# Performance work log

Measured on AMD Instinct MI355X. Metric: run time of the kernel, lower is better.

## Reference

```python
import jax, jax.numpy as jnp
import numpy as np

T = 2048        # tokens (single prefill sequence)
H = 4096        # hidden size
NQ = 32         # query heads
NKV = 8         # kv heads
HD = 128        # qk head_dim
VD = 96         # v head_dim (mismatched -> pad/slice path)
WIN = 1024      # sliding window size
E = 8           # routed experts
F = 1408        # moe intermediate
K = 2           # experts per token
EPS = 1e-6
THETA = 1e6


def setup_inputs() -> dict:
    key = jax.random.key(0)
    ks = jax.random.split(key, 10)
    s = 0.02
    return {
        "positions": jnp.arange(T, dtype=jnp.int32),
        "hidden_states": jax.random.normal(ks[0], (T, H), jnp.float32),
        "rms1_w": jnp.ones((H,), jnp.float32),
        "rms2_w": jnp.ones((H,), jnp.float32),
        "wq": jax.random.normal(ks[1], (H, NQ * HD), jnp.float32) * s,
        "wk": jax.random.normal(ks[2], (H, NKV * HD), jnp.float32) * s,
        "wv": jax.random.normal(ks[3], (H, NKV * VD), jnp.float32) * s,
        "wo": jax.random.normal(ks[4], (NQ * VD, H), jnp.float32) * s,
        "sink": jax.random.normal(ks[5], (NQ,), jnp.float32),
        "gate_w": jax.random.normal(ks[6], (H, E), jnp.float32) * s,
        "w_gate": jax.random.normal(ks[7], (E, H, F), jnp.float32) * s,
        "w_up": jax.random.normal(ks[8], (E, H, F), jnp.float32) * s,
        "w_down": jax.random.normal(ks[9], (E, F, H), jnp.float32) * s,
    }


def _rmsnorm(x, w):
    var = jnp.mean(x * x, axis=-1, keepdims=True)
    return x * jax.lax.rsqrt(var + EPS) * w


def _rope(positions, x):
    # neox style, full rotary over HD
    inv_freq = 1.0 / (THETA ** (jnp.arange(0, HD, 2, dtype=jnp.float32) / HD))
    ang = positions.astype(jnp.float32)[:, None] * inv_freq      # [T, HD/2]
    cos = jnp.cos(ang)[:, None, :]                               # [T, 1, HD/2]
    sin = jnp.sin(ang)[:, None, :]
    x1, x2 = x[..., : HD // 2], x[..., HD // 2 :]
    return jnp.concatenate([x1 * cos - x2 * sin, x2 * cos + x1 * sin], axis=-1)


def _forward(positions, hidden_states, rms1_w, rms2_w, wq, wk, wv, wo, sink,
             gate_w, w_gate, w_up, w_down):
    residual = hidden_states
    x = _rmsnorm(hidden_states, rms1_w)

    # ---- attention ----
    q = (x @ wq).reshape(T, NQ, HD)
    k = (x @ wk).reshape(T, NKV, HD)
    v = (x @ wv).reshape(T, NKV, VD)
    q = _rope(positions, q)
    k = _rope(positions, k)
    rep = NQ // NKV
    k = jnp.repeat(k, rep, axis=1)   # [T, NQ, HD]
    v = jnp.repeat(v, rep, axis=1)   # [T, NQ, VD]

    scale = HD ** -0.5
    scores = jnp.einsum('qhd,khd->hqk', q, k) * scale           # [NQ, T, T]
    i = positions[:, None]
    j = positions[None, :]
    mask = (j <= i) & ((i - j) < WIN)                            # causal + sliding window
    scores = jnp.where(mask[None, :, :], scores, jnp.float32(-1e30))
    # attention sink: extra per-head logit contributing only to the denominator
    sink_col = jnp.broadcast_to(sink[:, None, None], (NQ, T, 1))
    logits = jnp.concatenate([scores, sink_col], axis=-1)        # [NQ, T, T+1]
    probs = jax.nn.softmax(logits, axis=-1)[..., :T]
    attn = jnp.einsum('hqk,khv->qhv', probs, v)                  # [T, NQ, VD]
    attn_out = attn.reshape(T, NQ * VD) @ wo                     # [T, H]

    h = residual + attn_out

    # ---- MoE FFN ----
    x2 = _rmsnorm(h, rms2_w)
    router_logits = x2 @ gate_w                                   # [T, E]
    router_probs = jax.nn.softmax(router_logits, axis=-1)
    topk_w, topk_ids = jax.lax.top_k(router_probs, K)             # [T, K]
    topk_w = topk_w / jnp.sum(topk_w, axis=-1, keepdims=True)     # renormalize
    combine = jnp.zeros((T, E), jnp.float32).at[
        jnp.arange(T)[:, None], topk_ids].add(topk_w)             # [T, E]

    h1 = jnp.einsum('td,edf->etf', x2, w_gate)
    h2 = jnp.einsum('td,edf->etf', x2, w_up)
    eo = jnp.einsum('etf,efd->etd', jax.nn.silu(h1) * h2, w_down)  # [E, T, H]
    moe_out = jnp.einsum('etd,te->td', eo, combine)               # [T, H]

    return h + moe_out


def reference(positions, hidden_states, rms1_w, rms2_w, wq, wk, wv, wo, sink,
              gate_w, w_gate, w_up, w_down):
    return _forward(positions, hidden_states, rms1_w, rms2_w, wq, wk, wv, wo,
                    sink, gate_w, w_gate, w_up, w_down)
```

## Files before the change

kernel.cpp:

```cpp
#include <hip/hip_runtime.h>
#include <math.h>

#define T 2048
#define H 4096
#define NQ 32
#define NKV 8
#define HD 128
#define VD 96
#define WIN 1024
#define NE 8
#define FF 1408
#define TOPK 2

typedef __bf16 bf16x8 __attribute__((ext_vector_type(8)));
typedef unsigned short u16x8 __attribute__((ext_vector_type(8)));
typedef float f32x4 __attribute__((ext_vector_type(4)));
typedef unsigned short ushort_t;

__device__ __forceinline__ unsigned short f2bf(float f) {
  union { float f; unsigned u; } v; v.f = f;
  unsigned r = v.u + 0x7fffu + ((v.u >> 16) & 1u);
  return (unsigned short)(r >> 16);
}
__device__ __forceinline__ float bf2f(unsigned short h) {
  union { unsigned u; float f; } v; v.u = ((unsigned)h) << 16;
  return v.f;
}
__device__ __forceinline__ f32x4 mfma16(bf16x8 a, bf16x8 b, f32x4 c) {
  return __builtin_amdgcn_mfma_f32_16x16x32_bf16(a, b, c, 0, 0, 0);
}
__device__ __forceinline__ f32x4 fzero4() { f32x4 z = {0.f, 0.f, 0.f, 0.f}; return z; }

__device__ __forceinline__ void gl16(const void* g, void* l) {
  __builtin_amdgcn_global_load_lds(
      (const __attribute__((address_space(1))) void*)g,
      (__attribute__((address_space(3))) void*)l, 16, 0, 0);
}

template<int SPLITOUT>
__global__ __launch_bounds__(256) void tconv_kernel(
    const float* __restrict__ src, int ldsrc,
    ushort_t* __restrict__ dh, ushort_t* __restrict__ dl,
    int lddst, int dro, long long sE, long long dE)
{
  __shared__ float tile[64][65];
  int e = blockIdx.z;
  src += sE * (long long)e;
  dh += dE * (long long)e;
  if (SPLITOUT) dl += dE * (long long)e;
  int c0 = blockIdx.x * 64;
  int r0 = blockIdx.y * 64;
  int tid = threadIdx.x;
#pragma unroll
  for (int i = 0; i < 4; ++i) {
    int idx = tid + i * 256;
    int r = idx >> 4, c4 = (idx & 15) << 2;
    float4 v = *(const float4*)&src[(size_t)(r0 + r) * ldsrc + c0 + c4];
    tile[r][c4 + 0] = v.x; tile[r][c4 + 1] = v.y;
    tile[r][c4 + 2] = v.z; tile[r][c4 + 3] = v.w;
  }
  __syncthreads();
#pragma unroll
  for (int i = 0; i < 2; ++i) {
    int idx = tid + i * 256;
    int c = idx >> 3, r8 = (idx & 7) << 3;
    u16x8 hv, lv;
#pragma unroll
    for (int j = 0; j < 8; ++j) {
      float f = tile[r8 + j][c];
      unsigned short hh = f2bf(f);
      hv[j] = hh;
      if (SPLITOUT) lv[j] = f2bf(f - bf2f(hh));
    }
    size_t o = (size_t)(dro + c0 + c) * lddst + r0 + r8;
    *(u16x8*)&dh[o] = hv;
    if (SPLITOUT) *(u16x8*)&dl[o] = lv;
  }
}

template<int SPLIT, int GATHER, int EOFF, int OUTBF, int RES>
__global__ __launch_bounds__(256) void gemm_bt(
    const ushort_t* __restrict__ Ah, const ushort_t* __restrict__ Al, int lda,
    const ushort_t* __restrict__ Bh, const ushort_t* __restrict__ Bl,
    long long strideBe,
    void* __restrict__ Cp, int ldc,
    const float* __restrict__ res,
    const int* __restrict__ row_idx, const int* __restrict__ e_off,
    int M, int K)
{
  __shared__ __align__(16) ushort_t As[(SPLIT ? 2 : 1) * 4096];
  __shared__ __align__(16) ushort_t Bs[(SPLIT ? 2 : 1) * 4096];

  int rowbase = 0, Mloc = M;
  if (EOFF) {
    int e = blockIdx.z;
    rowbase = e_off[e];
    Mloc = e_off[e + 1] - rowbase;
    Bh += strideBe * (long long)e;
    if (SPLIT) Bl += strideBe * (long long)e;
  }
  int mtile = blockIdx.y * 128;
  if (mtile >= Mloc) return;
  int n0 = blockIdx.x * 128;

  int tid = threadIdx.x;
  int lane = tid & 63, wave = tid >> 6;
  int g = lane >> 4, cc = lane & 15;
  int wrow = (wave >> 1) * 64, wcol = (wave & 1) * 64;

  int ks = (tid & 3) << 3;
  const ushort_t *aph0, *aph1, *apl0 = nullptr, *apl1 = nullptr;
  {
    int r0 = (tid >> 2), r1 = (tid >> 2) + 64;
    long long ar0, ar1;
    if (EOFF || GATHER) {
      int g0 = mtile + r0; if (g0 >= Mloc) g0 = 0;
      int g1 = mtile + r1; if (g1 >= Mloc) g1 = 0;
      if (GATHER) { ar0 = row_idx[rowbase + g0]; ar1 = row_idx[rowbase + g1]; }
      else { ar0 = rowbase + g0; ar1 = rowbase + g1; }
    } else {
      ar0 = mtile + r0; ar1 = mtile + r1;
    }
    aph0 = Ah + ar0 * lda + ks;
    aph1 = Ah + ar1 * lda + ks;
    if (SPLIT) { apl0 = Al + ar0 * lda + ks; apl1 = Al + ar1 * lda + ks; }
  }
  const ushort_t* bph0 = Bh + (size_t)(n0 + (tid >> 2)) * K + ks;
  const ushort_t* bph1 = Bh + (size_t)(n0 + (tid >> 2) + 64) * K + ks;
  const ushort_t* bpl0 = SPLIT ? Bl + (size_t)(n0 + (tid >> 2)) * K + ks : nullptr;
  const ushort_t* bpl1 = SPLIT ? Bl + (size_t)(n0 + (tid >> 2) + 64) * K + ks : nullptr;
  ushort_t* la0 = As + tid * 8;
  ushort_t* la1 = As + (tid + 256) * 8;
  ushort_t* lb0 = Bs + tid * 8;
  ushort_t* lb1 = Bs + (tid + 256) * 8;

  f32x4 acc[4][4];
#pragma unroll
  for (int m = 0; m < 4; ++m)
#pragma unroll
    for (int n = 0; n < 4; ++n) acc[m][n] = fzero4();

  int nK = K >> 5;
  for (int kt = 0; kt < nK; ++kt) {
    int k0 = kt << 5;
    gl16(aph0 + k0, la0);
    gl16(aph1 + k0, la1);
    gl16(bph0 + k0, lb0);
    gl16(bph1 + k0, lb1);
    if (SPLIT) {
      gl16(apl0 + k0, la0 + 4096);
      gl16(apl1 + k0, la1 + 4096);
      gl16(bpl0 + k0, lb0 + 4096);
      gl16(bpl1 + k0, lb1 + 4096);
    }
    __syncthreads();
    bf16x8 avh[4], bvh[4], avl[4], bvl[4];
#pragma unroll
    for (int m = 0; m < 4; ++m) {
      int row = wrow + m * 16 + cc;
      avh[m] = *(const bf16x8*)&As[row * 32 + g * 8];
      if (SPLIT) avl[m] = *(const bf16x8*)&As[4096 + row * 32 + g * 8];
    }
#pragma unroll
    for (int n = 0; n < 4; ++n) {
      int row = wcol + n * 16 + cc;
      bvh[n] = *(const bf16x8*)&Bs[row * 32 + g * 8];
      if (SPLIT) bvl[n] = *(const bf16x8*)&Bs[4096 + row * 32 + g * 8];
    }
#pragma unroll
    for (int m = 0; m < 4; ++m)
#pragma unroll
      for (int n = 0; n < 4; ++n) {
        acc[m][n] = mfma16(avh[m], bvh[n], acc[m][n]);
        if (SPLIT) {
          acc[m][n] = mfma16(avh[m], bvl[n], acc[m][n]);
          acc[m][n] = mfma16(avl[m], bvh[n], acc[m][n]);
        }
      }
    __syncthreads();
  }

#pragma unroll
  for (int m = 0; m < 4; ++m) {
    int rl = wrow + m * 16 + g * 4;
#pragma unroll
    for (int n = 0; n < 4; ++n) {
      int col = n0 + wcol + n * 16 + cc;
#pragma unroll
      for (int r = 0; r < 4; ++r) {
        int grow = mtile + rl + r;
        if (grow < Mloc) {
          size_t off = (size_t)(rowbase + grow) * ldc + col;
          float vv = acc[m][n][r];
          if (OUTBF) {
            ((ushort_t*)Cp)[off] = f2bf(vv);
          } else {
            if (RES) vv += res[off];
            ((float*)Cp)[off] = vv;
          }
        }
      }
    }
  }
}

__global__ __launch_bounds__(256) void rmsnorm_hl_kernel(const float* __restrict__ in,
    const float* __restrict__ w, ushort_t* __restrict__ oh, ushort_t* __restrict__ ol)
{
  int t = blockIdx.x;
  int tid = threadIdx.x;
  const float4* rp = (const float4*)(in + (size_t)t * H);
  const float4* wp = (const float4*)w;
  float4 vv[4];
  float ss = 0.f;
#pragma unroll
  for (int i = 0; i < 4; ++i) {
    vv[i] = rp[tid + i * 256];
    ss += vv[i].x * vv[i].x + vv[i].y * vv[i].y + vv[i].z * vv[i].z + vv[i].w * vv[i].w;
  }
#pragma unroll
  for (int off = 32; off > 0; off >>= 1) ss += __shfl_xor(ss, off);
  __shared__ float red[4];
  if ((tid & 63) == 0) red[tid >> 6] = ss;
  __syncthreads();
  float tot = red[0] + red[1] + red[2] + red[3];
  float rs = rsqrtf(tot * (1.f / H) + 1e-6f);
#pragma unroll
  for (int i = 0; i < 4; ++i) {
    float4 x = vv[i];
    float4 ww = wp[tid + i * 256];
    float y0 = x.x * rs * ww.x, y1 = x.y * rs * ww.y;
    float y2 = x.z * rs * ww.z, y3 = x.w * rs * ww.w;
    ushort4 hh, ll;
    hh.x = f2bf(y0); hh.y = f2bf(y1); hh.z = f2bf(y2); hh.w = f2bf(y3);
    ll.x = f2bf(y0 - bf2f(hh.x)); ll.y = f2bf(y1 - bf2f(hh.y));
    ll.z = f2bf(y2 - bf2f(hh.z)); ll.w = f2bf(y3 - bf2f(hh.w));
    *(ushort4*)&oh[(size_t)t * H + (tid + i * 256) * 4] = hh;
    *(ushort4*)&ol[(size_t)t * H + (tid + i * 256) * 4] = ll;
  }
}

__global__ __launch_bounds__(256) void rmsnorm_fh_kernel(const float* __restrict__ in,
    const float* __restrict__ w, float* __restrict__ of, ushort_t* __restrict__ oh)
{
  int t = blockIdx.x;
  int tid = threadIdx.x;
  const float4* rp = (const float4*)(in + (size_t)t * H);
  const float4* wp = (const float4*)w;
  float4 vv[4];
  float ss = 0.f;
#pragma unroll
  for (int i = 0; i < 4; ++i) {
    vv[i] = rp[tid + i * 256];
    ss += vv[i].x * vv[i].x + vv[i].y * vv[i].y + vv[i].z * vv[i].z + vv[i].w * vv[i].w;
  }
#pragma unroll
  for (int off = 32; off > 0; off >>= 1) ss += __shfl_xor(ss, off);
  __shared__ float red[4];
  if ((tid & 63) == 0) red[tid >> 6] = ss;
  __syncthreads();
  float tot = red[0] + red[1] + red[2] + red[3];
  float rs = rsqrtf(tot * (1.f / H) + 1e-6f);
#pragma unroll
  for (int i = 0; i < 4; ++i) {
    float4 x = vv[i];
    float4 ww = wp[tid + i * 256];
    float4 o;
    o.x = x.x * rs * ww.x; o.y = x.y * rs * ww.y;
    o.z = x.z * rs * ww.z; o.w = x.w * rs * ww.w;
    *(float4*)&of[(size_t)t * H + (tid + i * 256) * 4] = o;
    ushort4 hh;
    hh.x = f2bf(o.x); hh.y = f2bf(o.y); hh.z = f2bf(o.z); hh.w = f2bf(o.w);
    *(ushort4*)&oh[(size_t)t * H + (tid + i * 256) * 4] = hh;
  }
}

__global__ __launch_bounds__(256) void rope_pack_kernel(const int* __restrict__ pos,
    const float* __restrict__ qkv,
    ushort_t* __restrict__ qh, ushort_t* __restrict__ ql,
    ushort_t* __restrict__ kh, ushort_t* __restrict__ kl,
    ushort_t* __restrict__ vh, ushort_t* __restrict__ vl)
{
  int t = blockIdx.x;
  float p = (float)pos[t];
  int tid = threadIdx.x;
  const float* row = qkv + (size_t)t * 5888;
  for (int idx = tid; idx < (NQ + NKV) * 64; idx += 256) {
    int col; ushort_t *dh, *dl; size_t dbase; int d;
    if (idx < NQ * 64) {
      int hh = idx >> 6; d = idx & 63;
      col = hh * HD + d;
      dbase = (size_t)t * (NQ * HD) + hh * HD;
      dh = qh; dl = ql;
    } else {
      int j = idx - NQ * 64;
      int hh = j >> 6; d = j & 63;
      col = 4096 + hh * HD + d;
      dbase = (size_t)t * (NKV * HD) + hh * HD;
      dh = kh; dl = kl;
    }
    float inv = exp2f(-19.931568569324174f * (float)(2 * d) * (1.0f / 128.0f));
    float ang = p * inv;
    float sn = sinf(ang), cs = cosf(ang);
    float x1 = row[col], x2 = row[col + 64];
    float o1 = x1 * cs - x2 * sn;
    float o2 = x2 * cs + x1 * sn;
    unsigned short h1 = f2bf(o1), h2 = f2bf(o2);
    dh[dbase + d] = h1; dl[dbase + d] = f2bf(o1 - bf2f(h1));
    dh[dbase + d + 64] = h2; dl[dbase + d + 64] = f2bf(o2 - bf2f(h2));
  }
  for (int idx = tid; idx < NKV * VD; idx += 256) {
    float v = row[5120 + idx];
    size_t o = (size_t)t * (NKV * VD) + idx;
    unsigned short hh = f2bf(v);
    vh[o] = hh; vl[o] = f2bf(v - bf2f(hh));
  }
}

__global__ __launch_bounds__(256) void attn_kernel(
    const ushort_t* __restrict__ qh, const ushort_t* __restrict__ ql,
    const ushort_t* __restrict__ kh, const ushort_t* __restrict__ kl,
    const ushort_t* __restrict__ vhp, const ushort_t* __restrict__ vlp,
    const float* __restrict__ sink, const int* __restrict__ pos,
    ushort_t* __restrict__ aoh, ushort_t* __restrict__ aol)
{
  __shared__ __align__(16) ushort_t Qs[2][64][136];
  __shared__ __align__(16) ushort_t Ks[2][32][136];
  __shared__ __align__(16) ushort_t Vt[2][96][40];
  __shared__ __align__(16) ushort_t Ps[2][4][16][40];
  __shared__ int posq[64];
  __shared__ int posk[32];

  const float SCALE = 0.08838834764831843f;
  int qs = blockIdx.x * 64;
  int head = blockIdx.y;
  int kvh = head >> 2;
  int tid = threadIdx.x;
  int lane = tid & 63, wave = tid >> 6;
  int g = lane >> 4, cc = lane & 15;
  int wq0 = wave * 16;

#pragma unroll
  for (int i = 0; i < 4; ++i) {
    int c = tid + i * 256;
    int row = c >> 4, ks = (c & 15) << 3;
    size_t gofs = (size_t)(qs + row) * (NQ * HD) + head * HD + ks;
    *(u16x8*)&Qs[0][row][ks] = *(const u16x8*)(qh + gofs);
    *(u16x8*)&Qs[1][row][ks] = *(const u16x8*)(ql + gofs);
  }
  if (tid < 64) posq[tid] = pos[qs + tid];

  float m_r[4], l_r[4];
  f32x4 acc_o[6];
#pragma unroll
  for (int r = 0; r < 4; ++r) { m_r[r] = -__builtin_huge_valf(); l_r[r] = 0.f; }
#pragma unroll
  for (int n = 0; n < 6; ++n) acc_o[n] = fzero4();

  int kstart = qs - (WIN - 1);
  if (kstart < 0) kstart = 0;
  kstart &= ~31;
  int kend = qs + 63;

  for (int k0 = kstart; k0 <= kend; k0 += 32) {
    __syncthreads();
#pragma unroll
    for (int i = 0; i < 2; ++i) {
      int c = tid + i * 256;
      int row = c >> 4, ks = (c & 15) << 3;
      size_t gofs = (size_t)(k0 + row) * (NKV * HD) + kvh * HD + ks;
      *(u16x8*)&Ks[0][row][ks] = *(const u16x8*)(kh + gofs);
      *(u16x8*)&Ks[1][row][ks] = *(const u16x8*)(kl + gofs);
    }
#pragma unroll
    for (int i = 0; i < 3; ++i) {
      int qd = tid + i * 256;
      int key = qd / 24, vq = qd % 24;
      size_t gofs = (size_t)(k0 + key) * (NKV * VD) + kvh * VD + vq * 4;
      ushort4 a = *(const ushort4*)(vhp + gofs);
      ushort4 b = *(const ushort4*)(vlp + gofs);
      Vt[0][vq * 4 + 0][key] = a.x; Vt[0][vq * 4 + 1][key] = a.y;
      Vt[0][vq * 4 + 2][key] = a.z; Vt[0][vq * 4 + 3][key] = a.w;
      Vt[1][vq * 4 + 0][key] = b.x; Vt[1][vq * 4 + 1][key] = b.y;
      Vt[1][vq * 4 + 2][key] = b.z; Vt[1][vq * 4 + 3][key] = b.w;
    }
    if (tid < 32) posk[tid] = pos[k0 + tid];
    __syncthreads();

    bf16x8 aqh[4], aql[4];
#pragma unroll
    for (int kk = 0; kk < 4; ++kk) {
      aqh[kk] = *(const bf16x8*)&Qs[0][wq0 + cc][kk * 32 + g * 8];
      aql[kk] = *(const bf16x8*)&Qs[1][wq0 + cc][kk * 32 + g * 8];
    }
    f32x4 sacc[2];
    sacc[0] = fzero4(); sacc[1] = fzero4();
#pragma unroll
    for (int kb = 0; kb < 2; ++kb)
#pragma unroll
      for (int kk = 0; kk < 4; ++kk) {
        bf16x8 bh = *(const bf16x8*)&Ks[0][kb * 16 + cc][kk * 32 + g * 8];
        bf16x8 bl = *(const bf16x8*)&Ks[1][kb * 16 + cc][kk * 32 + g * 8];
        sacc[kb] = mfma16(aqh[kk], bh, sacc[kb]);
        sacc[kb] = mfma16(aqh[kk], bl, sacc[kb]);
        sacc[kb] = mfma16(aql[kk], bh, sacc[kb]);
      }

    int j0 = posk[cc], j1 = posk[16 + cc];
#pragma unroll
    for (int r = 0; r < 4; ++r) {
      int irow = posq[wq0 + g * 4 + r];
      float s0 = sacc[0][r] * SCALE;
      float s1 = sacc[1][r] * SCALE;
      bool ok0 = (j0 <= irow) && (irow - j0 < WIN);
      bool ok1 = (j1 <= irow) && (irow - j1 < WIN);
      if (!ok0) s0 = -1e30f;
      if (!ok1) s1 = -1e30f;
      float rm = fmaxf(s0, s1);
#pragma unroll
      for (int off = 1; off < 16; off <<= 1) rm = fmaxf(rm, __shfl_xor(rm, off));
      float mn = fmaxf(m_r[r], rm);
      float p0 = ok0 ? __expf(s0 - mn) : 0.f;
      float p1 = ok1 ? __expf(s1 - mn) : 0.f;
      float rs = p0 + p1;
#pragma unroll
      for (int off = 1; off < 16; off <<= 1) rs += __shfl_xor(rs, off);
      float alpha = __expf(m_r[r] - mn);
      l_r[r] = l_r[r] * alpha + rs;
      m_r[r] = mn;
#pragma unroll
      for (int n = 0; n < 6; ++n) acc_o[n][r] *= alpha;
      unsigned short p0h = f2bf(p0), p1h = f2bf(p1);
      Ps[0][wave][g * 4 + r][cc] = p0h;
      Ps[1][wave][g * 4 + r][cc] = f2bf(p0 - bf2f(p0h));
      Ps[0][wave][g * 4 + r][16 + cc] = p1h;
      Ps[1][wave][g * 4 + r][16 + cc] = f2bf(p1 - bf2f(p1h));
    }
    bf16x8 pah = *(const bf16x8*)&Ps[0][wave][cc][g * 8];
    bf16x8 pal = *(const bf16x8*)&Ps[1][wave][cc][g * 8];
#pragma unroll
    for (int n = 0; n < 6; ++n) {
      bf16x8 bh = *(const bf16x8*)&Vt[0][n * 16 + cc][g * 8];
      bf16x8 bl = *(const bf16x8*)&Vt[1][n * 16 + cc][g * 8];
      acc_o[n] = mfma16(pah, bh, acc_o[n]);
      acc_o[n] = mfma16(pah, bl, acc_o[n]);
      acc_o[n] = mfma16(pal, bh, acc_o[n]);
    }
  }

  float snk = sink[head];
#pragma unroll
  for (int r = 0; r < 4; ++r) {
    float m2 = fmaxf(m_r[r], snk);
    float alpha = __expf(m_r[r] - m2);
    float denom = l_r[r] * alpha + __expf(snk - m2);
    float inv = 1.f / denom;
    int row = qs + wq0 + g * 4 + r;
#pragma unroll
    for (int n = 0; n < 6; ++n) {
      float val = acc_o[n][r] * alpha * inv;
      size_t off = (size_t)row * (NQ * VD) + head * VD + n * 16 + cc;
      unsigned short hh = f2bf(val);
      aoh[off] = hh;
      aol[off] = f2bf(val - bf2f(hh));
    }
  }
}

__global__ __launch_bounds__(64) void router_kernel(const float* __restrict__ x2,
    const float* __restrict__ gw, float* __restrict__ topkw, int* __restrict__ topkid)
{
  int t = blockIdx.x;
  int lane = threadIdx.x;
  float acc[NE];
#pragma unroll
  for (int e = 0; e < NE; ++e) acc[e] = 0.f;
  for (int hh = lane; hh < H; hh += 64) {
    float xv = x2[(size_t)t * H + hh];
    const float* g = gw + (size_t)hh * NE;
#pragma unroll
    for (int e = 0; e < NE; ++e) acc[e] = fmaf(xv, g[e], acc[e]);
  }
#pragma unroll
  for (int e = 0; e < NE; ++e)
#pragma unroll
    for (int off = 32; off > 0; off >>= 1) acc[e] += __shfl_xor(acc[e], off);
  if (lane == 0) {
    int b1 = 0; float v1 = acc[0];
#pragma unroll
    for (int e = 1; e < NE; ++e) { if (acc[e] > v1) { v1 = acc[e]; b1 = e; } }
    int b2 = -1; float v2 = -3.4e38f;
#pragma unroll
    for (int e = 0; e < NE; ++e) { if (e != b1 && acc[e] > v2) { v2 = acc[e]; b2 = e; } }
    float e2 = __expf(v2 - v1);
    float s = 1.f + e2;
    topkw[t * 2] = 1.f / s;
    topkw[t * 2 + 1] = e2 / s;
    topkid[t * 2] = b1;
    topkid[t * 2 + 1] = b2;
  }
}

__global__ __launch_bounds__(256) void route_build_kernel(
    const int* __restrict__ topkid, int* __restrict__ idssort,
    int* __restrict__ prow, int* __restrict__ eoffs)
{
  __shared__ int cnt[NE];
  __shared__ int off[NE + 1];
  __shared__ int cur[NE];
  int tid = threadIdx.x;
  if (tid < NE) cnt[tid] = 0;
  __syncthreads();
  for (int p = tid; p < T * TOPK; p += 256) atomicAdd(&cnt[topkid[p]], 1);
  __syncthreads();
  if (tid == 0) {
    off[0] = 0;
    for (int e = 0; e < NE; ++e) off[e + 1] = off[e] + cnt[e];
  }
  __syncthreads();
  if (tid < NE) cur[tid] = off[tid];
  __syncthreads();
  for (int p = tid; p < T * TOPK; p += 256) {
    int e = topkid[p];
    int ppos = atomicAdd(&cur[e], 1);
    idssort[ppos] = p >> 1;
    prow[p] = ppos;
  }
  if (tid <= NE) eoffs[tid] = off[tid];
}

__global__ __launch_bounds__(256) void silu_mul_kernel(
    const ushort_t* __restrict__ h12, ushort_t* __restrict__ oh)
{
  int id = blockIdx.x * 256 + threadIdx.x;
  int r = id / 176;
  int c8 = (id % 176) * 8;
  u16x8 a = *(const u16x8*)&h12[(size_t)r * 2816 + c8];
  u16x8 b = *(const u16x8*)&h12[(size_t)r * 2816 + 1408 + c8];
  u16x8 o;
#pragma unroll
  for (int j = 0; j < 8; ++j) {
    float x = bf2f(a[j]), y = bf2f(b[j]);
    float rr = x / (1.f + __expf(-x)) * y;
    o[j] = f2bf(rr);
  }
  *(u16x8*)&oh[(size_t)r * 1408 + c8] = o;
}

__global__ __launch_bounds__(256) void combine_kernel(const float* __restrict__ h,
    const float* __restrict__ eo, const float* __restrict__ topkw,
    const int* __restrict__ prow, float* __restrict__ out)
{
  int t = blockIdx.x, tid = threadIdx.x;
  float w0 = topkw[t * 2], w1 = topkw[t * 2 + 1];
  const float4* e0 = (const float4*)(eo + (size_t)prow[t * 2] * H);
  const float4* e1 = (const float4*)(eo + (size_t)prow[t * 2 + 1] * H);
  const float4* hp = (const float4*)(h + (size_t)t * H);
  float4* op = (float4*)(out + (size_t)t * H);
#pragma unroll
  for (int i = 0; i < 4; ++i) {
    int idx = tid + i * 256;
    float4 a = hp[idx], b = e0[idx], c = e1[idx];
    float4 o;
    o.x = a.x + w0 * b.x + w1 * c.x;
    o.y = a.y + w0 * b.y + w1 * c.y;
    o.z = a.z + w0 * b.z + w1 * c.z;
    o.w = a.w + w0 * b.w + w1 * c.w;
    op[idx] = o;
  }
}

extern "C" void kernel_launch(void* const* d_in, const int* in_sizes, int n_in,
                              void* d_out, int out_size, void* d_ws, size_t ws_size,
                              hipStream_t stream) {
  const int*   pos   = (const int*)d_in[0];
  const float* hid   = (const float*)d_in[1];
  const float* rms1w = (const float*)d_in[2];
  const float* rms2w = (const float*)d_in[3];
  const float* wq    = (const float*)d_in[4];
  const float* wk    = (const float*)d_in[5];
  const float* wv    = (const float*)d_in[6];
  const float* wo    = (const float*)d_in[7];
  const float* sink  = (const float*)d_in[8];
  const float* gw    = (const float*)d_in[9];
  const float* wgate = (const float*)d_in[10];
  const float* wup   = (const float*)d_in[11];
  const float* wdown = (const float*)d_in[12];
  float* out = (float*)d_out;

  const size_t MB = 1048576ull;
  if (ws_size < 462ull * MB) return;

  char* ws = (char*)d_ws;
  ushort_t* wqkvT_h = (ushort_t*)(ws + 0 * MB);
  ushort_t* wqkvT_l = (ushort_t*)(ws + 47 * MB);
  ushort_t* woT_h   = (ushort_t*)(ws + 94 * MB);
  ushort_t* woT_l   = (ushort_t*)(ws + 118 * MB);
  ushort_t* wgupT   = (ushort_t*)(ws + 0 * MB);
  ushort_t* wdownT  = (ushort_t*)(ws + 176 * MB);
  char* A0 = ws + 264 * MB;
  ushort_t* x1h = (ushort_t*)(A0 + 0 * MB);
  ushort_t* x1l = (ushort_t*)(A0 + 16 * MB);
  ushort_t* kh  = (ushort_t*)(A0 + 32 * MB);
  ushort_t* kl  = (ushort_t*)(A0 + 36 * MB);
  ushort_t* vh  = (ushort_t*)(A0 + 40 * MB);
  ushort_t* vl  = (ushort_t*)(A0 + 43 * MB);
  ushort_t* aoh = (ushort_t*)(A0 + 46 * MB);
  ushort_t* aol = (ushort_t*)(A0 + 58 * MB);
  ushort_t* qh  = (ushort_t*)(A0 + 0 * MB);
  ushort_t* ql  = (ushort_t*)(A0 + 16 * MB);
  float* eo   = (float*)(A0 + 0 * MB);
  float* qkvf = (float*)(A0 + 70 * MB);
  ushort_t* h12b = (ushort_t*)(A0 + 70 * MB);
  ushort_t* h1h  = (ushort_t*)(A0 + 93 * MB);
  float* h   = (float*)(A0 + 116 * MB);
  float* x2  = (float*)(A0 + 148 * MB);
  ushort_t* x2h = (ushort_t*)(A0 + 180 * MB);
  char* sm = A0 + 196 * MB;
  float* topkw  = (float*)(sm);
  int*  topkid  = (int*)(sm + 16384);
  int*  prow    = (int*)(sm + 32768);
  int*  idssort = (int*)(sm + 49152);
  int*  eoffs   = (int*)(sm + 65536);

  tconv_kernel<1><<<dim3(64, 64, 1), 256, 0, stream>>>(wq, 4096, wqkvT_h, wqkvT_l, 4096, 0, 0, 0);
  tconv_kernel<1><<<dim3(16, 64, 1), 256, 0, stream>>>(wk, 1024, wqkvT_h, wqkvT_l, 4096, 4096, 0, 0);
  tconv_kernel<1><<<dim3(12, 64, 1), 256, 0, stream>>>(wv, 768, wqkvT_h, wqkvT_l, 4096, 5120, 0, 0);
  tconv_kernel<1><<<dim3(64, 48, 1), 256, 0, stream>>>(wo, 4096, woT_h, woT_l, 3072, 0, 0, 0);
  tconv_kernel<0><<<dim3(64, 22, 8), 256, 0, stream>>>(wdown, 4096, wdownT, nullptr, 1408, 0,
      1408LL * 4096, 4096LL * 1408);

  rmsnorm_hl_kernel<<<T, 256, 0, stream>>>(hid, rms1w, x1h, x1l);

  gemm_bt<1, 0, 0, 0, 0><<<dim3(46, 16, 1), 256, 0, stream>>>(
      x1h, x1l, H, wqkvT_h, wqkvT_l, 0, qkvf, 5888, nullptr, nullptr, nullptr, T, H);

  rope_pack_kernel<<<T, 256, 0, stream>>>(pos, qkvf, qh, ql, kh, kl, vh, vl);

  attn_kernel<<<dim3(T / 64, NQ, 1), 256, 0, stream>>>(qh, ql, kh, kl, vh, vl,
      sink, pos, aoh, aol);

  gemm_bt<1, 0, 0, 0, 1><<<dim3(32, 16, 1), 256, 0, stream>>>(
      aoh, aol, NQ * VD, woT_h, woT_l, 0, h, H, hid, nullptr, nullptr, T, NQ * VD);

  rmsnorm_fh_kernel<<<T, 256, 0, stream>>>(h, rms2w, x2, x2h);

  router_kernel<<<T, 64, 0, stream>>>(x2, gw, topkw, topkid);
  route_build_kernel<<<1, 256, 0, stream>>>(topkid, idssort, prow, eoffs);

  tconv_kernel<0><<<dim3(22, 64, 8), 256, 0, stream>>>(wgate, 1408, wgupT, nullptr, 4096, 0,
      4096LL * 1408, 2816LL * 4096);
  tconv_kernel<0><<<dim3(22, 64, 8), 256, 0, stream>>>(wup, 1408, wgupT, nullptr, 4096, 1408,
      4096LL * 1408, 2816LL * 4096);
  gemm_bt<0, 1, 1, 1, 0><<<dim3(22, 32, 8), 256, 0, stream>>>(
      x2h, nullptr, H, wgupT, nullptr, 2816LL * 4096, h12b, 2816, nullptr, idssort, eoffs, 0, H);
  silu_mul_kernel<<<2816, 256, 0, stream>>>(h12b, h1h);
  gemm_bt<0, 0, 1, 0, 0><<<dim3(32, 32, 8), 256, 0, stream>>>(
      h1h, nullptr, FF, wdownT, nullptr, 4096LL * 1408, eo, H, nullptr, nullptr, eoffs, 0, FF);

  combine_kernel<<<T, 256, 0, stream>>>(h, eo, topkw, prow, out);
}
```

Measured before the change: 1.523 ms.

## Replace split-bf16 GEMM with K-concatenated operands and double-buffered swizzled pipeline

After: 1.525 ms. Within noise of the previous version (+0.1%).

```diff
diff --git a/kernel.cpp b/kernel.cpp
--- a/kernel.cpp
+++ b/kernel.cpp
@@ -37,102 +37,69 @@
       (__attribute__((address_space(3))) void*)l, 16, 0, 0);
 }
 
-template<int SPLITOUT>
-__global__ __launch_bounds__(256) void tconv_kernel(
-    const float* __restrict__ src, int ldsrc,
-    ushort_t* __restrict__ dh, ushort_t* __restrict__ dl,
-    int lddst, int dro, long long sE, long long dE)
-{
-  __shared__ float tile[64][65];
-  int e = blockIdx.z;
-  src += sE * (long long)e;
-  dh += dE * (long long)e;
-  if (SPLITOUT) dl += dE * (long long)e;
-  int c0 = blockIdx.x * 64;
-  int r0 = blockIdx.y * 64;
-  int tid = threadIdx.x;
-#pragma unroll
-  for (int i = 0; i < 4; ++i) {
-    int idx = tid + i * 256;
-    int r = idx >> 4, c4 = (idx & 15) << 2;
-    float4 v = *(const float4*)&src[(size_t)(r0 + r) * ldsrc + c0 + c4];
-    tile[r][c4 + 0] = v.x; tile[r][c4 + 1] = v.y;
-    tile[r][c4 + 2] = v.z; tile[r][c4 + 3] = v.w;
-  }
-  __syncthreads();
-#pragma unroll
-  for (int i = 0; i < 2; ++i) {
-    int idx = tid + i * 256;
-    int c = idx >> 3, r8 = (idx & 7) << 3;
-    u16x8 hv, lv;
-#pragma unroll
-    for (int j = 0; j < 8; ++j) {
-      float f = tile[r8 + j][c];
-      unsigned short hh = f2bf(f);
-      hv[j] = hh;
-      if (SPLITOUT) lv[j] = f2bf(f - bf2f(hh));
-    }
-    size_t o = (size_t)(dro + c0 + c) * lddst + r0 + r8;
-    *(u16x8*)&dh[o] = hv;
-    if (SPLITOUT) *(u16x8*)&dl[o] = lv;
-  }
-}
-
-template<int SPLIT, int GATHER, int EOFF, int OUTBF, int RES>
-__global__ __launch_bounds__(256) void gemm_bt(
-    const ushort_t* __restrict__ Ah, const ushort_t* __restrict__ Al, int lda,
-    const ushort_t* __restrict__ Bh, const ushort_t* __restrict__ Bl,
-    long long strideBe,
+template<int GATHER, int EOFF, int OUTBF, int RES>
+__global__ __launch_bounds__(256) void gemm8p(
+    const ushort_t* __restrict__ A, int lda,
+    const ushort_t* __restrict__ B, long long strideBe,
     void* __restrict__ Cp, int ldc,
     const float* __restrict__ res,
     const int* __restrict__ row_idx, const int* __restrict__ e_off,
     int M, int K)
 {
-  __shared__ __align__(16) ushort_t As[(SPLIT ? 2 : 1) * 4096];
-  __shared__ __align__(16) ushort_t Bs[(SPLIT ? 2 : 1) * 4096];
+  __shared__ __align__(16) ushort_t lds[32768];
 
   int rowbase = 0, Mloc = M;
   if (EOFF) {
     int e = blockIdx.z;
     rowbase = e_off[e];
     Mloc = e_off[e + 1] - rowbase;
-    Bh += strideBe * (long long)e;
-    if (SPLIT) Bl += strideBe * (long long)e;
+    B += strideBe * (long long)e;
   }
   int mtile = blockIdx.y * 128;
   if (mtile >= Mloc) return;
   int n0 = blockIdx.x * 128;
 
   int tid = threadIdx.x;
-  int lane = tid & 63, wave = tid >> 6;
-  int g = lane >> 4, cc = lane & 15;
-  int wrow = (wave >> 1) * 64, wcol = (wave & 1) * 64;
-
-  int ks = (tid & 3) << 3;
-  const ushort_t *aph0, *aph1, *apl0 = nullptr, *apl1 = nullptr;
+  int lane = tid & 63;
+  int wave = tid >> 6;
+  int wm = wave >> 1;
+  int wn = wave & 1;
+  int g  = lane >> 4;
+  int cc = lane & 15;
+  int gx = g ^ (cc & 3);
+
+  int aoff = (wm * 64 + cc) * 32 + gx * 8;
+  int boff = 16384 + (wn * 64 + cc) * 32 + gx * 8;
+
+  int r2 = tid >> 2;
+  int kx = ((tid & 3) ^ (r2 & 3)) * 8;
+  const ushort_t *pa0, *pa1;
   {
-    int r0 = (tid >> 2), r1 = (tid >> 2) + 64;
     long long ar0, ar1;
-    if (EOFF || GATHER) {
-      int g0 = mtile + r0; if (g0 >= Mloc) g0 = 0;
-      int g1 = mtile + r1; if (g1 >= Mloc) g1 = 0;
-      if (GATHER) { ar0 = row_idx[rowbase + g0]; ar1 = row_idx[rowbase + g1]; }
-      else { ar0 = rowbase + g0; ar1 = rowbase + g1; }
+    if (EOFF) {
+      int l0 = mtile + r2;       if (l0 > Mloc - 1) l0 = Mloc - 1;
+      int l1 = mtile + r2 + 64;  if (l1 > Mloc - 1) l1 = Mloc - 1;
+      if (GATHER) { ar0 = row_idx[rowbase + l0]; ar1 = row_idx[rowbase + l1]; }
+      else        { ar0 = rowbase + l0;          ar1 = rowbase + l1; }
     } else {
-      ar0 = mtile + r0; ar1 = mtile + r1;
-    }
-    aph0 = Ah + ar0 * lda + ks;
-    aph1 = Ah + ar1 * lda + ks;
-    if (SPLIT) { apl0 = Al + ar0 * lda + ks; apl1 = Al + ar1 * lda + ks; }
-  }
-  const ushort_t* bph0 = Bh + (size_t)(n0 + (tid >> 2)) * K + ks;
-  const ushort_t* bph1 = Bh + (size_t)(n0 + (tid >> 2) + 64) * K + ks;
-  const ushort_t* bpl0 = SPLIT ? Bl + (size_t)(n0 + (tid >> 2)) * K + ks : nullptr;
-  const ushort_t* bpl1 = SPLIT ? Bl + (size_t)(n0 + (tid >> 2) + 64) * K + ks : nullptr;
-  ushort_t* la0 = As + tid * 8;
-  ushort_t* la1 = As + (tid + 256) * 8;
-  ushort_t* lb0 = Bs + tid * 8;
-  ushort_t* lb1 = Bs + (tid + 256) * 8;
+      ar0 = mtile + r2; ar1 = mtile + r2 + 64;
+    }
+    pa0 = A + ar0 * (long long)lda + kx;
+    pa1 = A + ar1 * (long long)lda + kx;
+  }
+  const ushort_t* pb0 = B + (size_t)(n0 + r2) * K + kx;
+  const ushort_t* pb1 = B + (size_t)(n0 + r2 + 64) * K + kx;
+
+#define SA(slot, ks, kt) do {                                                  \
+    gl16(pa0 + (size_t)(kt) * 64 + (ks) * 32,                                  \
+         &lds[(slot) * 8192 + (ks) * 4096 + tid * 8]);                         \
+    gl16(pa1 + (size_t)(kt) * 64 + (ks) * 32,                                  \
+         &lds[(slot) * 8192 + (ks) * 4096 + tid * 8 + 2048]); } while (0)
+#define SB(slot, ks, kt) do {                                                  \
+    gl16(pb0 + (size_t)(kt) * 64 + (ks) * 32,                                  \
+         &lds[16384 + (slot) * 8192 + (ks) * 4096 + tid * 8]);                 \
+    gl16(pb1 + (size_t)(kt) * 64 + (ks) * 32,                                  \
+         &lds[16384 + (slot) * 8192 + (ks) * 4096 + tid * 8 + 2048]); } while (0)
 
   f32x4 acc[4][4];
 #pragma unroll
@@ -140,56 +107,64 @@
 #pragma unroll
     for (int n = 0; n < 4; ++n) acc[m][n] = fzero4();
 
-  int nK = K >> 5;
-  for (int kt = 0; kt < nK; ++kt) {
-    int k0 = kt << 5;
-    gl16(aph0 + k0, la0);
-    gl16(aph1 + k0, la1);
-    gl16(bph0 + k0, lb0);
-    gl16(bph1 + k0, lb1);
-    if (SPLIT) {
-      gl16(apl0 + k0, la0 + 4096);
-      gl16(apl1 + k0, la1 + 4096);
-      gl16(bpl0 + k0, lb0 + 4096);
-      gl16(bpl1 + k0, lb1 + 4096);
-    }
-    __syncthreads();
-    bf16x8 avh[4], bvh[4], avl[4], bvl[4];
-#pragma unroll
-    for (int m = 0; m < 4; ++m) {
-      int row = wrow + m * 16 + cc;
-      avh[m] = *(const bf16x8*)&As[row * 32 + g * 8];
-      if (SPLIT) avl[m] = *(const bf16x8*)&As[4096 + row * 32 + g * 8];
-    }
+  int NKT = K >> 6;
+  int NI = NKT >> 1;
+
+  SA(0, 0, 0); SB(0, 0, 0);
+  SA(0, 1, 0); SB(0, 1, 0);
+  SA(1, 0, 1); SB(1, 0, 1);
+  asm volatile("s_waitcnt vmcnt(4)" ::: "memory");
+  __builtin_amdgcn_s_barrier();
+  asm volatile("" ::: "memory");
+
+#define PH(slot, ks, STAGEOP, WAITOP)                                          \
+  {                                                                            \
+    bf16x8 a_[4], b_[4];                                                       \
+    _Pragma("unroll") for (int mm = 0; mm < 4; ++mm)                           \
+      a_[mm] = *(const bf16x8*)&lds[(slot) * 8192 + (ks) * 4096 + aoff + mm * 512]; \
+    _Pragma("unroll") for (int nn = 0; nn < 4; ++nn)                           \
+      b_[nn] = *(const bf16x8*)&lds[(slot) * 8192 + (ks) * 4096 + boff + nn * 512]; \
+    STAGEOP;                                                                   \
+    WAITOP;                                                                    \
+    asm volatile("" ::: "memory");                                             \
+    __builtin_amdgcn_s_barrier();                                              \
+    asm volatile("" ::: "memory");                                             \
+    __builtin_amdgcn_s_setprio(1);                                             \
+    _Pragma("unroll") for (int mm = 0; mm < 4; ++mm)                           \
+      _Pragma("unroll") for (int nn = 0; nn < 4; ++nn)                         \
+        acc[mm][nn] = mfma16(a_[mm], b_[nn], acc[mm][nn]);                     \
+    __builtin_amdgcn_s_setprio(0);                                             \
+    asm volatile("s_waitcnt lgkmcnt(0)" ::: "memory");                         \
+    __builtin_amdgcn_s_barrier();                                              \
+    asm volatile("" ::: "memory");                                             \
+  }
+
+  for (int i = 0; i < NI; ++i) {
+    int t1 = 2 * i + 1;
+    int t2 = 2 * i + 2; if (t2 > NKT - 1) t2 = NKT - 1;
+    int t3 = 2 * i + 3; if (t3 > NKT - 1) t3 = NKT - 1;
+    PH(0, 0, SA(1, 1, t1); SB(1, 1, t1), )
+    PH(0, 1, SA(0, 0, t2); SB(0, 0, t2),
+       asm volatile("s_waitcnt vmcnt(4)" ::: "memory"))
+    PH(1, 0, SA(0, 1, t2); SB(0, 1, t2), )
+    PH(1, 1, SA(1, 0, t3); SB(1, 0, t3),
+       asm volatile("s_waitcnt vmcnt(4)" ::: "memory"))
+  }
+#undef PH
+#undef SA
+#undef SB
+
+  int lr4 = (lane >> 4) * 4;
+#pragma unroll
+  for (int m = 0; m < 4; ++m) {
+    int rowl = mtile + wm * 64 + m * 16 + lr4;
 #pragma unroll
     for (int n = 0; n < 4; ++n) {
-      int row = wcol + n * 16 + cc;
-      bvh[n] = *(const bf16x8*)&Bs[row * 32 + g * 8];
-      if (SPLIT) bvl[n] = *(const bf16x8*)&Bs[4096 + row * 32 + g * 8];
-    }
-#pragma unroll
-    for (int m = 0; m < 4; ++m)
-#pragma unroll
-      for (int n = 0; n < 4; ++n) {
-        acc[m][n] = mfma16(avh[m], bvh[n], acc[m][n]);
-        if (SPLIT) {
-          acc[m][n] = mfma16(avh[m], bvl[n], acc[m][n]);
-          acc[m][n] = mfma16(avl[m], bvh[n], acc[m][n]);
-        }
-      }
-    __syncthreads();
-  }
-
-#pragma unroll
-  for (int m = 0; m < 4; ++m) {
-    int rl = wrow + m * 16 + g * 4;
-#pragma unroll
-    for (int n = 0; n < 4; ++n) {
-      int col = n0 + wcol + n * 16 + cc;
+      int col = n0 + wn * 64 + n * 16 + cc;
 #pragma unroll
       for (int r = 0; r < 4; ++r) {
-        int grow = mtile + rl + r;
-        if (grow < Mloc) {
+        int grow = rowl + r;
+        if (!EOFF || grow < Mloc) {
           size_t off = (size_t)(rowbase + grow) * ldc + col;
           float vv = acc[m][n][r];
           if (OUTBF) {
@@ -204,8 +179,86 @@
   }
 }
 
-__global__ __launch_bounds__(256) void rmsnorm_hl_kernel(const float* __restrict__ in,
-    const float* __restrict__ w, ushort_t* __restrict__ oh, ushort_t* __restrict__ ol)
+template<int SPLITOUT>
+__global__ __launch_bounds__(256) void tconv_kernel(
+    const float* __restrict__ src, int ldsrc,
+    ushort_t* __restrict__ dh, ushort_t* __restrict__ dl,
+    int lddst, int dro, long long sE, long long dE)
+{
+  __shared__ float tile[64][65];
+  int e = blockIdx.z;
+  src += sE * (long long)e;
+  dh += dE * (long long)e;
+  if (SPLITOUT) dl += dE * (long long)e;
+  int c0 = blockIdx.x * 64;
+  int r0 = blockIdx.y * 64;
+  int tid = threadIdx.x;
+#pragma unroll
+  for (int i = 0; i < 4; ++i) {
+    int idx = tid + i * 256;
+    int r = idx >> 4, c4 = (idx & 15) << 2;
+    float4 v = *(const float4*)&src[(size_t)(r0 + r) * ldsrc + c0 + c4];
+    tile[r][c4 + 0] = v.x; tile[r][c4 + 1] = v.y;
+    tile[r][c4 + 2] = v.z; tile[r][c4 + 3] = v.w;
+  }
+  __syncthreads();
+#pragma unroll
+  for (int i = 0; i < 2; ++i) {
+    int idx = tid + i * 256;
+    int c = idx >> 3, r8 = (idx & 7) << 3;
+    u16x8 hv, lv;
+#pragma unroll
+    for (int j = 0; j < 8; ++j) {
+      float f = tile[r8 + j][c];
+      unsigned short hh = f2bf(f);
+      hv[j] = hh;
+      if (SPLITOUT) lv[j] = f2bf(f - bf2f(hh));
+    }
+    size_t o = (size_t)(dro + c0 + c) * lddst + r0 + r8;
+    *(u16x8*)&dh[o] = hv;
+    if (SPLITOUT) *(u16x8*)&dl[o] = lv;
+  }
+}
+
+__global__ __launch_bounds__(256) void tconv_cat_kernel(
+    const float* __restrict__ src, int ldsrc,
+    ushort_t* __restrict__ dst, int lddst, int dro,
+    int kh1, int kh2, int klo)
+{
+  __shared__ float tile[64][65];
+  int c0 = blockIdx.x * 64;
+  int r0 = blockIdx.y * 64;
+  int tid = threadIdx.x;
+#pragma unroll
+  for (int i = 0; i < 4; ++i) {
+    int idx = tid + i * 256;
+    int r = idx >> 4, c4 = (idx & 15) << 2;
+    float4 v = *(const float4*)&src[(size_t)(r0 + r) * ldsrc + c0 + c4];
+    tile[r][c4 + 0] = v.x; tile[r][c4 + 1] = v.y;
+    tile[r][c4 + 2] = v.z; tile[r][c4 + 3] = v.w;
+  }
+  __syncthreads();
+#pragma unroll
+  for (int i = 0; i < 2; ++i) {
+    int idx = tid + i * 256;
+    int c = idx >> 3, r8 = (idx & 7) << 3;
+    u16x8 hv, lv;
+#pragma unroll
+    for (int j = 0; j < 8; ++j) {
+      float f = tile[r8 + j][c];
+      unsigned short hh = f2bf(f);
+      hv[j] = hh;
+      lv[j] = f2bf(f - bf2f(hh));
+    }
+    size_t o = (size_t)(dro + c0 + c) * lddst + r0 + r8;
+    *(u16x8*)&dst[o + kh1] = hv;
+    *(u16x8*)&dst[o + kh2] = hv;
+    *(u16x8*)&dst[o + klo] = lv;
+  }
+}
+
+__global__ __launch_bounds__(256) void rmsnorm_cat_kernel(const float* __restrict__ in,
+    const float* __restrict__ w, ushort_t* __restrict__ oc)
 {
   int t = blockIdx.x;
   int tid = threadIdx.x;
@@ -235,8 +288,10 @@
     hh.x = f2bf(y0); hh.y = f2bf(y1); hh.z = f2bf(y2); hh.w = f2bf(y3);
     ll.x = f2bf(y0 - bf2f(hh.x)); ll.y = f2bf(y1 - bf2f(hh.y));
     ll.z = f2bf(y2 - bf2f(hh.z)); ll.w = f2bf(y3 - bf2f(hh.w));
-    *(ushort4*)&oh[(size_t)t * H + (tid + i * 256) * 4] = hh;
-    *(ushort4*)&ol[(size_t)t * H + (tid + i * 256) * 4] = ll;
+    size_t base = (size_t)t * 12288 + (tid + i * 256) * 4;
+    *(ushort4*)&oc[base] = hh;
+    *(ushort4*)&oc[base + 4096] = ll;
+    *(ushort4*)&oc[base + 8192] = hh;
   }
 }
 
@@ -322,7 +377,7 @@
     const ushort_t* __restrict__ kh, const ushort_t* __restrict__ kl,
     const ushort_t* __restrict__ vhp, const ushort_t* __restrict__ vlp,
     const float* __restrict__ sink, const int* __restrict__ pos,
-    ushort_t* __restrict__ aoh, ushort_t* __restrict__ aol)
+    ushort_t* __restrict__ aocat)
 {
   __shared__ __align__(16) ushort_t Qs[2][64][136];
   __shared__ __align__(16) ushort_t Ks[2][32][136];
@@ -459,10 +514,12 @@
 #pragma unroll
     for (int n = 0; n < 6; ++n) {
       float val = acc_o[n][r] * alpha * inv;
-      size_t off = (size_t)row * (NQ * VD) + head * VD + n * 16 + cc;
+      size_t off = (size_t)row * 9216 + head * VD + n * 16 + cc;
       unsigned short hh = f2bf(val);
-      aoh[off] = hh;
-      aol[off] = f2bf(val - bf2f(hh));
+      unsigned short lo = f2bf(val - bf2f(hh));
+      aocat[off] = hh;
+      aocat[off + 3072] = lo;
+      aocat[off + 6144] = hh;
     }
   }
 }
@@ -592,71 +649,71 @@
   if (ws_size < 462ull * MB) return;
 
   char* ws = (char*)d_ws;
-  ushort_t* wqkvT_h = (ushort_t*)(ws + 0 * MB);
-  ushort_t* wqkvT_l = (ushort_t*)(ws + 47 * MB);
-  ushort_t* woT_h   = (ushort_t*)(ws + 94 * MB);
-  ushort_t* woT_l   = (ushort_t*)(ws + 118 * MB);
-  ushort_t* wgupT   = (ushort_t*)(ws + 0 * MB);
-  ushort_t* wdownT  = (ushort_t*)(ws + 176 * MB);
-  char* A0 = ws + 264 * MB;
-  ushort_t* x1h = (ushort_t*)(A0 + 0 * MB);
-  ushort_t* x1l = (ushort_t*)(A0 + 16 * MB);
-  ushort_t* kh  = (ushort_t*)(A0 + 32 * MB);
-  ushort_t* kl  = (ushort_t*)(A0 + 36 * MB);
-  ushort_t* vh  = (ushort_t*)(A0 + 40 * MB);
-  ushort_t* vl  = (ushort_t*)(A0 + 43 * MB);
-  ushort_t* aoh = (ushort_t*)(A0 + 46 * MB);
-  ushort_t* aol = (ushort_t*)(A0 + 58 * MB);
-  ushort_t* qh  = (ushort_t*)(A0 + 0 * MB);
-  ushort_t* ql  = (ushort_t*)(A0 + 16 * MB);
-  float* eo   = (float*)(A0 + 0 * MB);
-  float* qkvf = (float*)(A0 + 70 * MB);
-  ushort_t* h12b = (ushort_t*)(A0 + 70 * MB);
-  ushort_t* h1h  = (ushort_t*)(A0 + 93 * MB);
-  float* h   = (float*)(A0 + 116 * MB);
-  float* x2  = (float*)(A0 + 148 * MB);
-  ushort_t* x2h = (ushort_t*)(A0 + 180 * MB);
-  char* sm = A0 + 196 * MB;
+  ushort_t* wqkvTc = (ushort_t*)(ws + 0 * MB);
+  ushort_t* woTc   = (ushort_t*)(ws + 139 * MB);
+  ushort_t* wdownT = (ushort_t*)(ws + 211 * MB);
+  ushort_t* wgupT  = (ushort_t*)(ws + 0 * MB);
+  char* A0 = ws + 299 * MB;
+  float* h     = (float*)(A0 + 0 * MB);
+  ushort_t* x1cat = (ushort_t*)(A0 + 32 * MB);
+  ushort_t* qh  = (ushort_t*)(A0 + 32 * MB);
+  ushort_t* ql  = (ushort_t*)(A0 + 48 * MB);
+  ushort_t* kh  = (ushort_t*)(A0 + 64 * MB);
+  ushort_t* kl  = (ushort_t*)(A0 + 68 * MB);
+  ushort_t* vh  = (ushort_t*)(A0 + 72 * MB);
+  ushort_t* vl  = (ushort_t*)(A0 + 75 * MB);
+  float* qkvf  = (float*)(A0 + 80 * MB);
+  ushort_t* aocat = (ushort_t*)(A0 + 126 * MB);
+  ushort_t* x2h = (ushort_t*)(A0 + 96 * MB);
+  float* x2    = (float*)(A0 + 112 * MB);
+  ushort_t* h12b = (ushort_t*)(A0 + 112 * MB);
+  ushort_t* h1h  = (ushort_t*)(A0 + 134 * MB);
+  float* eo    = (float*)(A0 + 32 * MB);
+  char* sm = A0 + 162 * MB;
   float* topkw  = (float*)(sm);
   int*  topkid  = (int*)(sm + 16384);
   int*  prow    = (int*)(sm + 32768);
   int*  idssort = (int*)(sm + 49152);
   int*  eoffs   = (int*)(sm + 65536);
 
-  tconv_kernel<1><<<dim3(64, 64, 1), 256, 0, stream>>>(wq, 4096, wqkvT_h, wqkvT_l, 4096, 0, 0, 0);
-  tconv_kernel<1><<<dim3(16, 64, 1), 256, 0, stream>>>(wk, 1024, wqkvT_h, wqkvT_l, 4096, 4096, 0, 0);
-  tconv_kernel<1><<<dim3(12, 64, 1), 256, 0, stream>>>(wv, 768, wqkvT_h, wqkvT_l, 4096, 5120, 0, 0);
-  tconv_kernel<1><<<dim3(64, 48, 1), 256, 0, stream>>>(wo, 4096, woT_h, woT_l, 3072, 0, 0, 0);
-  tconv_kernel<0><<<dim3(64, 22, 8), 256, 0, stream>>>(wdown, 4096, wdownT, nullptr, 1408, 0,
-      1408LL * 4096, 4096LL * 1408);
-
-  rmsnorm_hl_kernel<<<T, 256, 0, stream>>>(hid, rms1w, x1h, x1l);
-
-  gemm_bt<1, 0, 0, 0, 0><<<dim3(46, 16, 1), 256, 0, stream>>>(
-      x1h, x1l, H, wqkvT_h, wqkvT_l, 0, qkvf, 5888, nullptr, nullptr, nullptr, T, H);
+  tconv_cat_kernel<<<dim3(64, 64, 1), 256, 0, stream>>>(wq, 4096, wqkvTc, 12288, 0,
+      0, 4096, 8192);
+  tconv_cat_kernel<<<dim3(16, 64, 1), 256, 0, stream>>>(wk, 1024, wqkvTc, 12288, 4096,
+      0, 4096, 8192);
+  tconv_cat_kernel<<<dim3(12, 64, 1), 256, 0, stream>>>(wv, 768, wqkvTc, 12288, 5120,
+      0, 4096, 8192);
+  tconv_cat_kernel<<<dim3(64, 48, 1), 256, 0, stream>>>(wo, 4096, woTc, 9216, 0,
+      0, 3072, 6144);
+  tconv_kernel<0><<<dim3(64, 22, 8), 256, 0, stream>>>(wdown, 4096, wdownT, nullptr,
+      1408, 0, 1408LL * 4096, 4096LL * 1408);
+
+  rmsnorm_cat_kernel<<<T, 256, 0, stream>>>(hid, rms1w, x1cat);
+
+  gemm8p<0, 0, 0, 0><<<dim3(46, 16, 1), 256, 0, stream>>>(
+      x1cat, 12288, wqkvTc, 0, qkvf, 5888, nullptr, nullptr, nullptr, T, 12288);
 
   rope_pack_kernel<<<T, 256, 0, stream>>>(pos, qkvf, qh, ql, kh, kl, vh, vl);
 
   attn_kernel<<<dim3(T / 64, NQ, 1), 256, 0, stream>>>(qh, ql, kh, kl, vh, vl,
-      sink, pos, aoh, aol);
-
-  gemm_bt<1, 0, 0, 0, 1><<<dim3(32, 16, 1), 256, 0, stream>>>(
-      aoh, aol, NQ * VD, woT_h, woT_l, 0, h, H, hid, nullptr, nullptr, T, NQ * VD);
+      sink, pos, aocat);
+
+  gemm8p<0, 0, 0, 1><<<dim3(32, 16, 1), 256, 0, stream>>>(
+      aocat, 9216, woTc, 0, h, H, hid, nullptr, nullptr, T, 9216);
 
   rmsnorm_fh_kernel<<<T, 256, 0, stream>>>(h, rms2w, x2, x2h);
 
   router_kernel<<<T, 64, 0, stream>>>(x2, gw, topkw, topkid);
   route_build_kernel<<<1, 256, 0, stream>>>(topkid, idssort, prow, eoffs);
 
-  tconv_kernel<0><<<dim3(22, 64, 8), 256, 0, stream>>>(wgate, 1408, wgupT, nullptr, 4096, 0,
-      4096LL * 1408, 2816LL * 4096);
-  tconv_kernel<0><<<dim3(22, 64, 8), 256, 0, stream>>>(wup, 1408, wgupT, nullptr, 4096, 1408,
-      4096LL * 1408, 2816LL * 4096);
-  gemm_bt<0, 1, 1, 1, 0><<<dim3(22, 32, 8), 256, 0, stream>>>(
-      x2h, nullptr, H, wgupT, nullptr, 2816LL * 4096, h12b, 2816, nullptr, idssort, eoffs, 0, H);
+  tconv_kernel<0><<<dim3(22, 64, 8), 256, 0, stream>>>(wgate, 1408, wgupT, nullptr,
+      4096, 0, 4096LL * 1408, 2816LL * 4096);
+  tconv_kernel<0><<<dim3(22, 64, 8), 256, 0, stream>>>(wup, 1408, wgupT, nullptr,
+      4096, 1408, 4096LL * 1408, 2816LL * 4096);
+  gemm8p<1, 1, 1, 0><<<dim3(22, 32, 8), 256, 0, stream>>>(
+      x2h, 4096, wgupT, 2816LL * 4096, h12b, 2816, nullptr, idssort, eoffs, 0, 4096);
   silu_mul_kernel<<<2816, 256, 0, stream>>>(h12b, h1h);
-  gemm_bt<0, 0, 1, 0, 0><<<dim3(32, 32, 8), 256, 0, stream>>>(
-      h1h, nullptr, FF, wdownT, nullptr, 4096LL * 1408, eo, H, nullptr, nullptr, eoffs, 0, FF);
+  gemm8p<0, 1, 0, 0><<<dim3(32, 32, 8), 256, 0, stream>>>(
+      h1h, 1408, wdownT, 4096LL * 1408, eo, H, nullptr, nullptr, eoffs, 0, 1408);
 
   combine_kernel<<<T, 256, 0, stream>>>(h, eo, topkw, prow, out);
 }
```
